# Performance work log

Measured on AMD Instinct MI355X. Metric: run time of the kernel, lower is better.

## Reference

```python
import jax, jax.numpy as jnp
import numpy as np

C = 256   # in_channels
H = 48
W = 48
B = 2     # batch after chunking into 3 frames; input batch = 3*B
F = 3     # frames (torch.chunk(x, 3))
G = 4     # GroupNorm groups
EPS = 1e-6


def setup_inputs() -> dict:
    key = jax.random.key(0)
    ks = jax.random.split(key, 10)
    s = C ** -0.5  # keep q/k magnitudes sane so softmax is not saturated
    return {
        "x":    jax.random.normal(ks[0], (F * B, C, H, W), jnp.float32),
        "gn_w": jnp.ones((C,), jnp.float32),
        "gn_b": jnp.zeros((C,), jnp.float32),
        "wq":   jax.random.normal(ks[1], (C, C), jnp.float32) * s,
        "bq":   jax.random.normal(ks[2], (C,), jnp.float32) * 0.02,
        "wk":   jax.random.normal(ks[3], (C, C), jnp.float32) * s,
        "bk":   jax.random.normal(ks[4], (C,), jnp.float32) * 0.02,
        "wv":   jax.random.normal(ks[5], (C, C), jnp.float32) * s,
        "bv":   jax.random.normal(ks[6], (C,), jnp.float32) * 0.02,
        "wp":   jax.random.normal(ks[7], (C, C), jnp.float32) * s,
        "bp":   jax.random.normal(ks[8], (C,), jnp.float32) * 0.02,
    }


def reference(x, gn_w, gn_b, wq, bq, wk, bk, wv, bv, wp, bp):
    B3, c, h, w = x.shape
    b = B3 // F
    # torch.chunk(x, 3) + stack(dim=2) -> (b, c, f, h, w); chunk index is frame
    hx = jnp.moveaxis(x.reshape(F, b, c, h, w), 0, 2)  # (b, c, f, h, w)

    # GroupNorm(num_groups=4, eps=1e-6, affine)
    hg = hx.reshape(b, G, c // G, F, h, w)
    mu = hg.mean(axis=(2, 3, 4, 5), keepdims=True)
    var = hg.var(axis=(2, 3, 4, 5), keepdims=True)
    hn = ((hg - mu) * jax.lax.rsqrt(var + EPS)).reshape(b, c, F, h, w)
    hn = hn * gn_w[None, :, None, None, None] + gn_b[None, :, None, None, None]

    # 1x1x1 Conv3d == channel matmul over flattened tokens n = (f h w)
    n = F * h * w
    hf = hn.reshape(b, c, n)                                  # (b, c, n)
    q = jnp.einsum('oc,bcn->bon', wq, hf) + bq[None, :, None]
    k = jnp.einsum('oc,bcn->bon', wk, hf) + bk[None, :, None]
    v = jnp.einsum('oc,bcn->bon', wv, hf) + bv[None, :, None]

    # scores[b,n,m] = sum_c q[b,c,n] * k[b,c,m], scaled by c^-0.5, softmax over m
    scores = jnp.einsum('bcn,bcm->bnm', q, k) * (c ** -0.5)
    attn = jax.nn.softmax(scores, axis=-1)                    # (b, n, n)

    # out[b,c,n] = sum_m v[b,c,m] * attn[b,n,m]
    o = jnp.einsum('bcm,bnm->bcn', v, attn)
    o = jnp.einsum('oc,bcn->bon', wp, o) + bp[None, :, None]  # proj_out

    o = o.reshape(b, c, F, h, w)
    # permute(0,2,1,3,4) then merge (b f) -> batch (b-major, f-minor)
    o = jnp.moveaxis(o, 2, 1).reshape(B3, c, h, w)
    return x + o
```

## Files before the change

kernel.cpp:

```cpp
#include <hip/hip_runtime.h>
#include <stdint.h>

#define CDIM 256
#define HW 2304
#define FR 3
#define NBATCH 2
#define NTOK 6912
#define EPSV 1e-6f
#define QSCALE (0.0625f * 1.44269504088896f)

typedef __attribute__((ext_vector_type(8))) short short8;
typedef __attribute__((ext_vector_type(4))) short short4v;
typedef __attribute__((ext_vector_type(4))) float f32x4;
typedef unsigned short u16;

__device__ inline u16 f2bf(float f) {
  union { float f; uint32_t u; } v; v.f = f;
  uint32_t r = v.u + 0x7FFFu + ((v.u >> 16) & 1u);
  return (u16)(r >> 16);
}
__device__ inline float bf2f(u16 h) {
  union { uint32_t u; float f; } v; v.u = ((uint32_t)h) << 16; return v.f;
}
__device__ inline void gload16(const void* g, void* l) {
  __builtin_amdgcn_global_load_lds(
      (const __attribute__((address_space(1))) void*)g,
      (__attribute__((address_space(3))) void*)l, 16, 0, 0);
}

__global__ void pre_k(const float* x, float* part, const float* wq,
                      const float* wk, const float* wv, const float* wp,
                      u16* wb) {
  if (blockIdx.x >= 256) {
    int idx = (blockIdx.x - 256) * 256 + threadIdx.x;
    wb[0 * 65536 + idx] = f2bf(wq[idx] * QSCALE);
    wb[1 * 65536 + idx] = f2bf(wk[idx]);
    wb[2 * 65536 + idx] = f2bf(wv[idx]);
    wb[3 * 65536 + idx] = f2bf(wp[idx]);
    return;
  }
  int bg = blockIdx.x >> 5, sl = blockIdx.x & 31;
  int b = bg >> 2, g = bg & 3;
  int tid = threadIdx.x;
  float s1 = 0.f, s2 = 0.f;
  for (int i = tid; i < 2 * NTOK; i += 256) {
    int cl = sl * 2 + (i / NTOK); int rem = i % NTOK;
    int f = rem / HW; int hw = rem - f * HW;
    float v = x[((size_t)(f * NBATCH + b) * CDIM + g * 64 + cl) * HW + hw];
    s1 += v; s2 += v * v;
  }
  #pragma unroll
  for (int m = 32; m >= 1; m >>= 1) {
    s1 += __shfl_xor(s1, m, 64);
    s2 += __shfl_xor(s2, m, 64);
  }
  __shared__ float r1[4], r2[4];
  int wid = tid >> 6;
  if ((tid & 63) == 0) { r1[wid] = s1; r2[wid] = s2; }
  __syncthreads();
  if (tid == 0) {
    part[blockIdx.x * 2 + 0] = r1[0] + r1[1] + r1[2] + r1[3];
    part[blockIdx.x * 2 + 1] = r2[0] + r2[1] + r2[2] + r2[3];
  }
}

__global__ void gn_fin_k(const float* part, float* stats) {
  int tid = threadIdx.x;
  if (tid < 8) {
    float s1 = 0.f, s2 = 0.f;
    for (int s = 0; s < 32; ++s) {
      s1 += part[(tid * 32 + s) * 2 + 0];
      s2 += part[(tid * 32 + s) * 2 + 1];
    }
    float inv = 1.f / (64.f * NTOK);
    float mu = s1 * inv;
    float var = s2 * inv - mu * mu;
    stats[tid * 2 + 0] = mu;
    stats[tid * 2 + 1] = rsqrtf(var + EPSV);
  }
}

__global__ void gn_apply_k(const float* x, const float* gn_w, const float* gn_b,
                           const float* stats, u16* hn) {
  int nt = blockIdx.x, ct = blockIdx.y, b = blockIdx.z;
  int tid = threadIdx.x;
  __shared__ float tile[64][65];
  int n0 = nt * 64; int f = n0 / HW; int hw0 = n0 - f * HW;
  float mu = stats[(b * 4 + ct) * 2 + 0];
  float rs = stats[(b * 4 + ct) * 2 + 1];
  #pragma unroll
  for (int i = 0; i < 16; ++i) {
    int lin = i * 256 + tid;
    int cr = lin >> 6, nc = lin & 63;
    int c = ct * 64 + cr;
    float v = x[((size_t)(f * NBATCH + b) * CDIM + c) * HW + hw0 + nc];
    tile[cr][nc] = (v - mu) * rs * gn_w[c] + gn_b[c];
  }
  __syncthreads();
  #pragma unroll
  for (int i = 0; i < 16; ++i) {
    int lin = i * 256 + tid;
    int nr = lin >> 6, cc = lin & 63;
    hn[((size_t)b * NTOK + n0 + nr) * CDIM + ct * 64 + cc] = f2bf(tile[cc][nr]);
  }
}

__global__ __launch_bounds__(256) void qkv_k(const u16* hn, const u16* wb,
    const float* bq, const float* bk, const float* bv,
    u16* qb, u16* kb, u16* vb) {
  int nt = blockIdx.x;
  int op = blockIdx.y >> 1, b = blockIdx.y & 1;
  int tid = threadIdx.x, lane = tid & 63, wid = tid >> 6;
  int lr = lane & 15, lg = lane >> 4;
  __shared__ __align__(16) char hn_lds[32768];
  {
    const char* src = (const char*)(hn + ((size_t)b * NTOK + nt * 64) * CDIM);
    #pragma unroll
    for (int i = 0; i < 8; ++i) {
      int off = i * 4096 + wid * 1024 + lane * 16;
      int row = off >> 9;
      gload16(src + (off ^ ((row & 7) << 4)), hn_lds + i * 4096 + wid * 1024);
    }
  }
  __syncthreads();
  f32x4 acc[16];
  #pragma unroll
  for (int i = 0; i < 16; ++i) acc[i] = (f32x4){0.f, 0.f, 0.f, 0.f};
  const u16* wsrc = wb + op * 65536;
  __builtin_amdgcn_s_setprio(1);
  #pragma unroll
  for (int cc = 0; cc < 4; ++cc) {
    short8 afr[2];
    #pragma unroll
    for (int kc = 0; kc < 2; ++kc) {
      int row = wid * 16 + lr;
      int byte = row * 512 + (cc * 64 + kc * 32 + lg * 8) * 2;
      afr[kc] = *(const short8*)(hn_lds + (byte ^ ((row & 7) << 4)));
    }
    #pragma unroll
    for (int cot = 0; cot < 16; ++cot) {
      #pragma unroll
      for (int kc = 0; kc < 2; ++kc) {
        short8 bfr = *(const short8*)(wsrc + (size_t)(cot * 16 + lr) * CDIM +
                                      cc * 64 + kc * 32 + lg * 8);
        if (op == 2)
          acc[cot] = __builtin_amdgcn_mfma_f32_16x16x32_bf16(afr[kc], bfr, acc[cot], 0, 0, 0);
        else
          acc[cot] = __builtin_amdgcn_mfma_f32_16x16x32_bf16(bfr, afr[kc], acc[cot], 0, 0, 0);
      }
    }
  }
  __builtin_amdgcn_s_setprio(0);
  if (op == 2) {
    int m0 = wid * 16 + lg * 4;
    char* vtile = (char*)vb + (size_t)b * NTOK * CDIM * 2 + (size_t)nt * 32768;
    #pragma unroll
    for (int cot = 0; cot < 16; ++cot) {
      int co = cot * 16 + lr;
      float bb = bv[co];
      short4v r;
      #pragma unroll
      for (int j = 0; j < 4; ++j) r[j] = (short)f2bf(acc[cot][j] + bb);
      int slot = ((m0 >> 3) + co) & 7;
      *(short4v*)(vtile + co * 128 + slot * 16 + (m0 & 7) * 2) = r;
    }
  } else {
    int row = wid * 16 + lr;
    int n = nt * 64 + row;
    const float* bias = (op == 0) ? bq : bk;
    float bscale = (op == 0) ? QSCALE : 1.0f;
    char* ktile = (char*)kb + (size_t)b * NTOK * CDIM * 2 + (size_t)nt * 32768;
    #pragma unroll
    for (int cot = 0; cot < 16; ++cot) {
      int co = cot * 16 + lg * 4;
      f32x4 b4 = *(const f32x4*)(bias + co);
      short4v r;
      #pragma unroll
      for (int j = 0; j < 4; ++j) r[j] = (short)f2bf(acc[cot][j] + b4[j] * bscale);
      if (op == 0) {
        *(short4v*)(qb + ((size_t)b * NTOK + n) * CDIM + co) = r;
      } else {
        int slot = ((co >> 3) + 2 * row) & 31;
        *(short4v*)(ktile + row * 512 + slot * 16 + (co & 7) * 2) = r;
      }
    }
  }
}

template <bool SPLIT>
__global__ __launch_bounds__(768, 3) void flash_k(const u16* qb, const u16* kb,
                                                  const u16* vb, u16* opart,
                                                  float* ml, u16* ob) {
  int qt = blockIdx.x, b = blockIdx.y, sp = blockIdx.z;
  int tid = threadIdx.x, lane = tid & 63, wid = tid >> 6;
  int lr = lane & 15, lg = lane >> 4;
  __shared__ __align__(16) char k_lds[2][32768];
  __shared__ __align__(16) char v_lds[2][32768];
  __shared__ __align__(16) char p_lds[12][2048];

  int t0 = SPLIT ? 36 * sp : 0;
  int t1 = SPLIT ? 36 * sp + 36 : 108;

  short8 aq[8];
  int nq = qt * 192 + wid * 16 + lr;
  const u16* qsrc = qb + ((size_t)b * NTOK + nq) * CDIM;
  #pragma unroll
  for (int kc = 0; kc < 8; ++kc) aq[kc] = *(const short8*)(qsrc + kc * 32 + lg * 8);

  float mrun = -1e30f, lrun = 0.f;
  f32x4 acc[16];
  #pragma unroll
  for (int i = 0; i < 16; ++i) acc[i] = (f32x4){0.f, 0.f, 0.f, 0.f};

  const char* kbb = (const char*)(kb + (size_t)b * NTOK * CDIM);
  const char* vbb = (const char*)(vb + (size_t)b * NTOK * CDIM);
  char* pw = p_lds[wid];

  {
    const char* ks = kbb + (size_t)t0 * 32768;
    const char* vs = vbb + (size_t)t0 * 32768;
    for (int ch = wid; ch < 64; ch += 12) {
      if (ch < 32) gload16(ks + ch * 1024 + lane * 16, k_lds[0] + ch * 1024);
      else gload16(vs + (ch - 32) * 1024 + lane * 16, v_lds[0] + (ch - 32) * 1024);
    }
  }
  __syncthreads();

  for (int t = t0; t < t1; ++t) {
    int cur = (t - t0) & 1;
    if (t + 1 < t1) {
      const char* ks = kbb + (size_t)(t + 1) * 32768;
      const char* vs = vbb + (size_t)(t + 1) * 32768;
      for (int ch = wid; ch < 64; ch += 12) {
        if (ch < 32) gload16(ks + ch * 1024 + lane * 16, k_lds[cur ^ 1] + ch * 1024);
        else gload16(vs + (ch - 32) * 1024 + lane * 16, v_lds[cur ^ 1] + (ch - 32) * 1024);
      }
    }
    f32x4 s[4];
    __builtin_amdgcn_s_setprio(1);
    #pragma unroll
    for (int mt = 0; mt < 4; ++mt) {
      f32x4 a = (f32x4){0.f, 0.f, 0.f, 0.f};
      #pragma unroll
      for (int kc = 0; kc < 8; ++kc) {
        int row = mt * 16 + lr;
        int slot = (kc * 4 + lg + 2 * row) & 31;
        short8 kf = *(const short8*)(k_lds[cur] + row * 512 + slot * 16);
        a = __builtin_amdgcn_mfma_f32_16x16x32_bf16(kf, aq[kc], a, 0, 0, 0);
      }
      s[mt] = a;
    }
    __builtin_amdgcn_s_setprio(0);
    float m0 = fmaxf(fmaxf(s[0][0], s[0][1]), fmaxf(s[0][2], s[0][3]));
    float m1 = fmaxf(fmaxf(s[1][0], s[1][1]), fmaxf(s[1][2], s[1][3]));
    float m2 = fmaxf(fmaxf(s[2][0], s[2][1]), fmaxf(s[2][2], s[2][3]));
    float m3 = fmaxf(fmaxf(s[3][0], s[3][1]), fmaxf(s[3][2], s[3][3]));
    float pmax = fmaxf(fmaxf(m0, m1), fmaxf(m2, m3));
    pmax = fmaxf(pmax, __shfl_xor(pmax, 16, 64));
    pmax = fmaxf(pmax, __shfl_xor(pmax, 32, 64));
    if (__any(pmax > mrun + 6.0f)) {
      float mn = fmaxf(mrun, pmax);
      float r = exp2f(mrun - mn);
      mrun = mn; lrun *= r;
      #pragma unroll
      for (int i = 0; i < 16; ++i) {
        acc[i][0] *= r; acc[i][1] *= r; acc[i][2] *= r; acc[i][3] *= r;
      }
    }
    float ls = 0.f;
    #pragma unroll
    for (int mt = 0; mt < 4; ++mt) {
      #pragma unroll
      for (int j = 0; j < 4; ++j) {
        float p = exp2f(s[mt][j] - mrun);
        s[mt][j] = p;
        ls += p;
      }
    }
    ls += __shfl_xor(ls, 16, 64);
    ls += __shfl_xor(ls, 32, 64);
    lrun += ls;
    #pragma unroll
    for (int mt = 0; mt < 4; ++mt) {
      #pragma unroll
      for (int tp = 0; tp < 2; ++tp) {
        uint32_t pk = (uint32_t)f2bf(s[mt][2 * tp]) |
                      ((uint32_t)f2bf(s[mt][2 * tp + 1]) << 16);
        int byte = lr * 128 + mt * 32 + lg * 8 + tp * 4;
        *(uint32_t*)(pw + (byte ^ ((lr & 7) << 4))) = pk;
      }
    }
    __builtin_amdgcn_s_setprio(1);
    #pragma unroll
    for (int mc = 0; mc < 2; ++mc) {
      int pb = lr * 128 + mc * 64 + lg * 16;
      short8 bfr = *(const short8*)(pw + (pb ^ ((lr & 7) << 4)));
      #pragma unroll
      for (int ct = 0; ct < 16; ++ct) {
        int row = ct * 16 + lr;
        int slot = (mc * 4 + lg + row) & 7;
        short8 av = *(const short8*)(v_lds[cur] + row * 128 + slot * 16);
        acc[ct] = __builtin_amdgcn_mfma_f32_16x16x32_bf16(av, bfr, acc[ct], 0, 0, 0);
      }
    }
    __builtin_amdgcn_s_setprio(0);
    __syncthreads();
  }

  if (!SPLIT) {
    float linv = 1.0f / lrun;
    u16* d0 = ob + ((size_t)b * NTOK + nq) * CDIM;
    #pragma unroll
    for (int ct = 0; ct < 16; ++ct) {
      short4v r;
      #pragma unroll
      for (int j = 0; j < 4; ++j) r[j] = (short)f2bf(acc[ct][j] * linv);
      *(short4v*)(d0 + ct * 16 + lg * 4) = r;
    }
  } else {
    u16* d0 = opart + ((size_t)(sp * 2 + b) * NTOK + nq) * CDIM;
    #pragma unroll
    for (int ct = 0; ct < 16; ++ct) {
      short4v r;
      #pragma unroll
      for (int j = 0; j < 4; ++j) r[j] = (short)f2bf(acc[ct][j]);
      *(short4v*)(d0 + ct * 16 + lg * 4) = r;
    }
    if (lg == 0) {
      size_t mb = (size_t)(sp * 2 + b) * 2;
      ml[(mb + 0) * NTOK + nq] = mrun;
      ml[(mb + 1) * NTOK + nq] = lrun;
    }
  }
}

__global__ __launch_bounds__(256) void comb_k(const u16* opart, const float* ml,
                                              u16* ob) {
  int nt = blockIdx.x, b = blockIdx.y;
  int tid = threadIdx.x;
  #pragma unroll
  for (int g = 0; g < 8; ++g) {
    int n = nt * 64 + g * 8 + (tid >> 5);
    int c0 = (tid & 31) * 8;
    float m[3], l[3];
    #pragma unroll
    for (int s = 0; s < 3; ++s) {
      m[s] = ml[((size_t)(s * 2 + b) * 2 + 0) * NTOK + n];
      l[s] = ml[((size_t)(s * 2 + b) * 2 + 1) * NTOK + n];
    }
    float M = fmaxf(fmaxf(m[0], m[1]), m[2]);
    float w[3]; float den = 0.f;
    #pragma unroll
    for (int s = 0; s < 3; ++s) { w[s] = exp2f(m[s] - M); den += w[s] * l[s]; }
    float inv = 1.f / den;
    float o[8] = {0.f, 0.f, 0.f, 0.f, 0.f, 0.f, 0.f, 0.f};
    #pragma unroll
    for (int s = 0; s < 3; ++s) {
      short8 v = *(const short8*)(opart + ((size_t)(s * 2 + b) * NTOK + n) * CDIM + c0);
      #pragma unroll
      for (int j = 0; j < 8; ++j) o[j] += w[s] * bf2f((u16)v[j]);
    }
    short8 r8;
    #pragma unroll
    for (int j = 0; j < 8; ++j) r8[j] = (short)f2bf(o[j] * inv);
    *(short8*)(ob + ((size_t)b * NTOK + n) * CDIM + c0) = r8;
  }
}

__global__ __launch_bounds__(256) void proj_k(const u16* ob, const u16* wb,
    const float* bp, const float* x, float* out) {
  int nt = blockIdx.x, b = blockIdx.y, z = blockIdx.z;
  int tid = threadIdx.x, lane = tid & 63, wid = tid >> 6;
  int lr = lane & 15, lg = lane >> 4;
  __shared__ __align__(16) char o_lds[32768];
  const u16* wpb = wb + 3 * 65536;
  {
    const char* src = (const char*)(ob + ((size_t)b * NTOK + nt * 64) * CDIM);
    #pragma unroll
    for (int i = 0; i < 8; ++i) {
      int off = i * 4096 + wid * 1024 + lane * 16;
      int row = off >> 9;
      gload16(src + (off ^ ((row & 7) << 4)), o_lds + i * 4096 + wid * 1024);
    }
  }
  __syncthreads();
  #pragma unroll
  for (int ct2 = 0; ct2 < 2; ++ct2) {
    int cot = z * 8 + wid * 2 + ct2;
    short8 aw[8];
    #pragma unroll
    for (int kc = 0; kc < 8; ++kc)
      aw[kc] = *(const short8*)(wpb + (size_t)(cot * 16 + lr) * CDIM + kc * 32 + lg * 8);
    #pragma unroll
    for (int ntile = 0; ntile < 4; ++ntile) {
      f32x4 a = (f32x4){0.f, 0.f, 0.f, 0.f};
      #pragma unroll
      for (int kc = 0; kc < 8; ++kc) {
        int row = ntile * 16 + lr;
        int byte = row * 512 + (kc * 32 + lg * 8) * 2;
        short8 bfr = *(const short8*)(o_lds + (byte ^ ((row & 7) << 4)));
        a = __builtin_amdgcn_mfma_f32_16x16x32_bf16(aw[kc], bfr, a, 0, 0, 0);
      }
      int n = nt * 64 + ntile * 16 + lr;
      int f = n / HW; int hw = n - f * HW;
      #pragma unroll
      for (int j = 0; j < 4; ++j) {
        int co = cot * 16 + lg * 4 + j;
        float val = a[j] + bp[co];
        size_t oi = ((size_t)(b * FR + f) * CDIM + co) * HW + hw;
        out[oi] = x[oi] + val;
      }
    }
  }
}

extern "C" void kernel_launch(void* const* d_in, const int* in_sizes, int n_in,
                              void* d_out, int out_size, void* d_ws, size_t ws_size,
                              hipStream_t stream) {
  const float* x    = (const float*)d_in[0];
  const float* gn_w = (const float*)d_in[1];
  const float* gn_b = (const float*)d_in[2];
  const float* wq   = (const float*)d_in[3];
  const float* bq   = (const float*)d_in[4];
  const float* wk   = (const float*)d_in[5];
  const float* bk   = (const float*)d_in[6];
  const float* wv   = (const float*)d_in[7];
  const float* bv   = (const float*)d_in[8];
  const float* wp   = (const float*)d_in[9];
  const float* bp   = (const float*)d_in[10];
  float* out = (float*)d_out;
  char* ws = (char*)d_ws;

  float* stats = (float*)(ws + 0);
  float* part  = (float*)(ws + 256);
  u16* wb = (u16*)(ws + 4096);
  u16* hn = (u16*)(ws + 528384);
  u16* qb = (u16*)(ws + 7606272);
  u16* kb = (u16*)(ws + 14684160);
  u16* vb = (u16*)(ws + 21762048);
  u16* ob = (u16*)(ws + 28839936);
  u16* opart = (u16*)(ws + 35917824);
  float* ml  = (float*)(ws + 57151488);
  const size_t NEED_SPLIT = 57483264;

  pre_k<<<512, 256, 0, stream>>>(x, part, wq, wk, wv, wp, wb);
  gn_fin_k<<<1, 64, 0, stream>>>(part, stats);
  gn_apply_k<<<dim3(108, 4, 2), 256, 0, stream>>>(x, gn_w, gn_b, stats, hn);
  qkv_k<<<dim3(108, 6), 256, 0, stream>>>(hn, wb, bq, bk, bv, qb, kb, vb);
  if (ws_size >= NEED_SPLIT) {
    flash_k<true><<<dim3(36, 2, 3), 768, 0, stream>>>(qb, kb, vb, opart, ml, ob);
    comb_k<<<dim3(108, 2), 256, 0, stream>>>(opart, ml, ob);
  } else {
    flash_k<false><<<dim3(36, 2, 1), 768, 0, stream>>>(qb, kb, vb, opart, ml, ob);
  }
  proj_k<<<dim3(108, 2, 2), 256, 0, stream>>>(ob, wb, bp, x, out);
}
```

Baseline: 229.3 us.

## Fuse split-softmax combine into projection and relayout K/V tiles for direct LDS reads

The K and V tiles are stored in a chunk-major layout so flash_k can address LDS fragments with constant offsets instead of computing XOR-swizzled slots. Bf16 packing of probabilities now uses the hardware v_cvt_pk_bf16_f32 instruction. The separate comb_k kernel is folded into proj_k, which merges the three partial outputs straight into LDS. Each proj block now handles all 256 output channels instead of half, removing one launch and the round trip of ob through global memory. The new K/V layout may cause LDS bank conflicts, and the proj grid is half as large.

```diff
diff --git a/kernel.cpp b/kernel.cpp
--- a/kernel.cpp
+++ b/kernel.cpp
@@ -154,6 +154,7 @@
   if (op == 2) {
     int m0 = wid * 16 + lg * 4;
     char* vtile = (char*)vb + (size_t)b * NTOK * CDIM * 2 + (size_t)nt * 32768;
+    int mchunk = (m0 >> 3);
     #pragma unroll
     for (int cot = 0; cot < 16; ++cot) {
       int co = cot * 16 + lr;
@@ -161,8 +162,7 @@
       short4v r;
       #pragma unroll
       for (int j = 0; j < 4; ++j) r[j] = (short)f2bf(acc[cot][j] + bb);
-      int slot = ((m0 >> 3) + co) & 7;
-      *(short4v*)(vtile + co * 128 + slot * 16 + (m0 & 7) * 2) = r;
+      *(short4v*)(vtile + mchunk * 4096 + co * 16 + (lg & 1) * 8) = r;
     }
   } else {
     int row = wid * 16 + lr;
@@ -180,8 +180,8 @@
       if (op == 0) {
         *(short4v*)(qb + ((size_t)b * NTOK + n) * CDIM + co) = r;
       } else {
-        int slot = ((co >> 3) + 2 * row) & 31;
-        *(short4v*)(ktile + row * 512 + slot * 16 + (co & 7) * 2) = r;
+        int colchunk = cot * 2 + (lg >> 1);
+        *(short4v*)(ktile + colchunk * 1024 + row * 16 + (lg & 1) * 8) = r;
       }
     }
   }
@@ -215,6 +215,8 @@
   const char* kbb = (const char*)(kb + (size_t)b * NTOK * CDIM);
   const char* vbb = (const char*)(vb + (size_t)b * NTOK * CDIM);
   char* pw = p_lds[wid];
+  int kqoff = lg * 1024 + lr * 16;
+  int pvoff = lg * 4096 + lr * 16;
 
   {
     const char* ks = kbb + (size_t)t0 * 32768;
@@ -236,6 +238,8 @@
         else gload16(vs + (ch - 32) * 1024 + lane * 16, v_lds[cur ^ 1] + (ch - 32) * 1024);
       }
     }
+    const char* kcur = k_lds[cur] + kqoff;
+    const char* vcur = v_lds[cur] + pvoff;
     f32x4 s[4];
     __builtin_amdgcn_s_setprio(1);
     #pragma unroll
@@ -243,9 +247,7 @@
       f32x4 a = (f32x4){0.f, 0.f, 0.f, 0.f};
       #pragma unroll
       for (int kc = 0; kc < 8; ++kc) {
-        int row = mt * 16 + lr;
-        int slot = (kc * 4 + lg + 2 * row) & 31;
-        short8 kf = *(const short8*)(k_lds[cur] + row * 512 + slot * 16);
+        short8 kf = *(const short8*)(kcur + kc * 4096 + mt * 256);
         a = __builtin_amdgcn_mfma_f32_16x16x32_bf16(kf, aq[kc], a, 0, 0, 0);
       }
       s[mt] = a;
@@ -284,8 +286,9 @@
     for (int mt = 0; mt < 4; ++mt) {
       #pragma unroll
       for (int tp = 0; tp < 2; ++tp) {
-        uint32_t pk = (uint32_t)f2bf(s[mt][2 * tp]) |
-                      ((uint32_t)f2bf(s[mt][2 * tp + 1]) << 16);
+        uint32_t pk;
+        asm("v_cvt_pk_bf16_f32 %0, %1, %2"
+            : "=v"(pk) : "v"(s[mt][2 * tp]), "v"(s[mt][2 * tp + 1]));
         int byte = lr * 128 + mt * 32 + lg * 8 + tp * 4;
         *(uint32_t*)(pw + (byte ^ ((lr & 7) << 4))) = pk;
       }
@@ -297,9 +300,7 @@
       short8 bfr = *(const short8*)(pw + (pb ^ ((lr & 7) << 4)));
       #pragma unroll
       for (int ct = 0; ct < 16; ++ct) {
-        int row = ct * 16 + lr;
-        int slot = (mc * 4 + lg + row) & 7;
-        short8 av = *(const short8*)(v_lds[cur] + row * 128 + slot * 16);
+        short8 av = *(const short8*)(vcur + mc * 16384 + ct * 256);
         acc[ct] = __builtin_amdgcn_mfma_f32_16x16x32_bf16(av, bfr, acc[ct], 0, 0, 0);
       }
     }
@@ -334,47 +335,45 @@
   }
 }
 
-__global__ __launch_bounds__(256) void comb_k(const u16* opart, const float* ml,
-                                              u16* ob) {
+template <bool SPLIT>
+__global__ __launch_bounds__(256) void proj_k(const u16* ob, const u16* opart,
+    const float* ml, const u16* wb, const float* bp, const float* x, float* out) {
   int nt = blockIdx.x, b = blockIdx.y;
-  int tid = threadIdx.x;
-  #pragma unroll
-  for (int g = 0; g < 8; ++g) {
-    int n = nt * 64 + g * 8 + (tid >> 5);
-    int c0 = (tid & 31) * 8;
-    float m[3], l[3];
-    #pragma unroll
-    for (int s = 0; s < 3; ++s) {
-      m[s] = ml[((size_t)(s * 2 + b) * 2 + 0) * NTOK + n];
-      l[s] = ml[((size_t)(s * 2 + b) * 2 + 1) * NTOK + n];
-    }
-    float M = fmaxf(fmaxf(m[0], m[1]), m[2]);
-    float w[3]; float den = 0.f;
-    #pragma unroll
-    for (int s = 0; s < 3; ++s) { w[s] = exp2f(m[s] - M); den += w[s] * l[s]; }
-    float inv = 1.f / den;
-    float o[8] = {0.f, 0.f, 0.f, 0.f, 0.f, 0.f, 0.f, 0.f};
-    #pragma unroll
-    for (int s = 0; s < 3; ++s) {
-      short8 v = *(const short8*)(opart + ((size_t)(s * 2 + b) * NTOK + n) * CDIM + c0);
-      #pragma unroll
-      for (int j = 0; j < 8; ++j) o[j] += w[s] * bf2f((u16)v[j]);
-    }
-    short8 r8;
-    #pragma unroll
-    for (int j = 0; j < 8; ++j) r8[j] = (short)f2bf(o[j] * inv);
-    *(short8*)(ob + ((size_t)b * NTOK + n) * CDIM + c0) = r8;
-  }
-}
-
-__global__ __launch_bounds__(256) void proj_k(const u16* ob, const u16* wb,
-    const float* bp, const float* x, float* out) {
-  int nt = blockIdx.x, b = blockIdx.y, z = blockIdx.z;
   int tid = threadIdx.x, lane = tid & 63, wid = tid >> 6;
   int lr = lane & 15, lg = lane >> 4;
   __shared__ __align__(16) char o_lds[32768];
   const u16* wpb = wb + 3 * 65536;
-  {
+  if (SPLIT) {
+    #pragma unroll
+    for (int i = 0; i < 8; ++i) {
+      int off = i * 4096 + tid * 16;
+      int row = off >> 9;
+      int c0 = (off & 511) >> 1;
+      int n = nt * 64 + row;
+      float mm[3], llv[3];
+      #pragma unroll
+      for (int s = 0; s < 3; ++s) {
+        mm[s] = ml[((size_t)(s * 2 + b) * 2 + 0) * NTOK + n];
+        llv[s] = ml[((size_t)(s * 2 + b) * 2 + 1) * NTOK + n];
+      }
+      float M = fmaxf(fmaxf(mm[0], mm[1]), mm[2]);
+      float w[3]; float den = 0.f;
+      #pragma unroll
+      for (int s = 0; s < 3; ++s) { w[s] = exp2f(mm[s] - M); den += w[s] * llv[s]; }
+      float inv = 1.f / den;
+      float o[8] = {0.f, 0.f, 0.f, 0.f, 0.f, 0.f, 0.f, 0.f};
+      #pragma unroll
+      for (int s = 0; s < 3; ++s) {
+        short8 v = *(const short8*)(opart + ((size_t)(s * 2 + b) * NTOK + n) * CDIM + c0);
+        #pragma unroll
+        for (int j = 0; j < 8; ++j) o[j] += w[s] * bf2f((u16)v[j]);
+      }
+      short8 r8;
+      #pragma unroll
+      for (int j = 0; j < 8; ++j) r8[j] = (short)f2bf(o[j] * inv);
+      *(short8*)(o_lds + (off ^ ((row & 7) << 4))) = r8;
+    }
+  } else {
     const char* src = (const char*)(ob + ((size_t)b * NTOK + nt * 64) * CDIM);
     #pragma unroll
     for (int i = 0; i < 8; ++i) {
@@ -385,8 +384,8 @@
   }
   __syncthreads();
   #pragma unroll
-  for (int ct2 = 0; ct2 < 2; ++ct2) {
-    int cot = z * 8 + wid * 2 + ct2;
+  for (int ct2 = 0; ct2 < 4; ++ct2) {
+    int cot = wid * 4 + ct2;
     short8 aw[8];
     #pragma unroll
     for (int kc = 0; kc < 8; ++kc)
@@ -449,9 +448,9 @@
   qkv_k<<<dim3(108, 6), 256, 0, stream>>>(hn, wb, bq, bk, bv, qb, kb, vb);
   if (ws_size >= NEED_SPLIT) {
     flash_k<true><<<dim3(36, 2, 3), 768, 0, stream>>>(qb, kb, vb, opart, ml, ob);
-    comb_k<<<dim3(108, 2), 256, 0, stream>>>(opart, ml, ob);
+    proj_k<true><<<dim3(108, 2), 256, 0, stream>>>(ob, opart, ml, wb, bp, x, out);
   } else {
     flash_k<false><<<dim3(36, 2, 1), 768, 0, stream>>>(qb, kb, vb, opart, ml, ob);
-  }
-  proj_k<<<dim3(108, 2, 2), 256, 0, stream>>>(ob, wb, bp, x, out);
-}
+    proj_k<false><<<dim3(108, 2), 256, 0, stream>>>(ob, opart, ml, wb, bp, x, out);
+  }
+}
```

Result: no change. 227.2 us (-0.9%).
